# Performance work log

Hardware: AMD Instinct MI355X
Metric: run time of the kernel (lower is better)

Reference implementation:

```python
import jax, jax.numpy as jnp
import numpy as np

N, K, FC, FX, E = 16384, 16, 2, 32, 256


def _lin_init(key, fin, fout):
    kw, kb = jax.random.split(key)
    s = 1.0 / np.sqrt(fin)
    W = jax.random.uniform(kw, (fin, fout), jnp.float32, -s, s)
    b = jax.random.uniform(kb, (fout,), jnp.float32, -s, s)
    return W, b


def setup_inputs() -> dict:
    key = jax.random.key(0)
    ks = jax.random.split(key, 13)
    c = jax.random.uniform(ks[0], (N, FC), jnp.float32)
    x = jax.random.normal(ks[1], (N, FX), jnp.float32)
    W_coords, b_coords = _lin_init(ks[2], FC, E)
    W_attri, b_attri = _lin_init(ks[3], FX, E)
    W_g1, b_g1 = _lin_init(ks[4], FC, E)
    W_g2, b_g2 = _lin_init(ks[5], E, E)
    W_g3, b_g3 = _lin_init(ks[6], E, E)
    W_f1, b_f1 = _lin_init(ks[7], FX, E)
    W_f2, b_f2 = _lin_init(ks[8], E, E)
    W_f3, b_f3 = _lin_init(ks[9], E, E)
    W_d1, b_d1 = _lin_init(ks[10], 2 * E, 2 * E)
    W_d2, b_d2 = _lin_init(ks[11], 2 * E, 2)
    return dict(c=c, x=x,
                W_coords=W_coords, b_coords=b_coords,
                W_attri=W_attri, b_attri=b_attri,
                W_g1=W_g1, b_g1=b_g1, W_g2=W_g2, b_g2=b_g2, W_g3=W_g3, b_g3=b_g3,
                W_f1=W_f1, b_f1=b_f1, W_f2=W_f2, b_f2=b_f2, W_f3=W_f3, b_f3=b_f3,
                W_d1=W_d1, b_d1=b_d1, W_d2=W_d2, b_d2=b_d2)


def knn_edges(c, k):
    # PyG knn_graph (loop=False, flow='source_to_target'):
    # edge_index[0]=neighbor(src), edge_index[1]=node(dst).
    n = c.shape[0]
    sq = jnp.sum(c * c, axis=1)
    d2 = sq[:, None] + sq[None, :] - 2.0 * (c @ c.T)  # [N,N] squared dists
    d2 = d2.at[jnp.arange(n), jnp.arange(n)].set(jnp.inf)  # exclude self
    _, idx = jax.lax.top_k(-d2, k)  # [N,k] nearest neighbor indices
    src = idx.reshape(-1)
    dst = jnp.repeat(jnp.arange(n), k)
    return src, dst


def gcn_conv(h, src, dst, ew, W, b):
    # PyG GCNConv: linear -> add self-loops (weight 1) -> sym norm -> scatter-add -> +bias
    n = h.shape[0]
    hw = h @ W
    loop = jnp.arange(n)
    s = jnp.concatenate([src, loop])
    d = jnp.concatenate([dst, loop])
    w = jnp.concatenate([ew, jnp.ones((n,), h.dtype)])
    deg = jax.ops.segment_sum(w, d, num_segments=n)
    dinv = jnp.where(deg > 0, jax.lax.rsqrt(deg), 0.0)
    norm = dinv[s] * w * dinv[d]
    out = jax.ops.segment_sum(norm[:, None] * hw[s], d, num_segments=n)
    return out + b


def reference(c, x, W_coords, b_coords, W_attri, b_attri,
              W_g1, b_g1, W_g2, b_g2, W_g3, b_g3,
              W_f1, b_f1, W_f2, b_f2, W_f3, b_f3,
              W_d1, b_d1, W_d2, b_d2):
    src, dst = knn_edges(c, K)
    dist = jnp.linalg.norm(c[src] - c[dst], axis=1)
    ew = jnp.exp(-dist / 2.0)
    ew = jnp.where(ew > 10.0, 0.0, ew)  # faithful to source (never triggers)

    coords0 = c @ W_coords + b_coords
    attri0 = x @ W_attri + b_attri

    # eval mode: dropout is identity
    g1 = jax.nn.relu(gcn_conv(c, src, dst, ew, W_g1, b_g1))
    m1 = jax.nn.relu(x @ W_f1 + b_f1)
    g1 = coords0 + g1
    m1 = attri0 + m1

    g2 = jax.nn.relu(gcn_conv(g1, src, dst, ew, W_g2, b_g2))
    m2 = jax.nn.relu(m1 @ W_f2 + b_f2)
    g2 = g1 + g2
    m2 = m1 + m2

    g3 = jax.nn.relu(gcn_conv(g2, src, dst, ew, W_g3, b_g3))
    m3 = jax.nn.relu(m2 @ W_f3 + b_f3)
    g3 = g2 + g3
    m3 = m2 + m3

    combined = jnp.concatenate([g3, m3], axis=1)
    out = jax.nn.relu(combined @ W_d1 + b_d1) @ W_d2 + b_d2
    mean = out[:, 0]
    sigma = 0.2 + 0.8 * jax.nn.softplus(out[:, 1])
    return mean.reshape(-1, 1), sigma.reshape(-1, 1), g3, m3
```

## Files before the change

kernel.cpp:

```cpp
#include <hip/hip_runtime.h>
#include <math.h>

#define NPTS 16384
#define KNN 16
#define GRES 128
#define NCELL (GRES * GRES)

typedef unsigned long long ull;
typedef __attribute__((ext_vector_type(8))) short  bf16x8;
typedef __attribute__((ext_vector_type(4))) float  f32x4;

__device__ inline unsigned short f2bf(float f) {
    unsigned int u = __float_as_uint(f);
    u += 0x7fffu + ((u >> 16) & 1u);
    return (unsigned short)(u >> 16);
}
__device__ inline float bf2f(unsigned short u) {
    return __uint_as_float(((unsigned int)u) << 16);
}

__global__ __launch_bounds__(256) void grid_count_kernel(const float2* __restrict__ c,
    int* __restrict__ cnt)
{
    const int i = blockIdx.x * 256 + threadIdx.x;
    float2 p = c[i];
    int cx = min(GRES - 1, max(0, (int)(p.x * GRES)));
    int cy = min(GRES - 1, max(0, (int)(p.y * GRES)));
    atomicAdd(&cnt[cy * GRES + cx], 1);
}

__global__ __launch_bounds__(256) void scan_p1_kernel(const int* __restrict__ cnt,
    int* __restrict__ bsum)
{
    __shared__ int red[256];
    const int t = threadIdx.x;
    red[t] = cnt[blockIdx.x * 256 + t];
    __syncthreads();
    for (int s = 128; s > 0; s >>= 1) { if (t < s) red[t] += red[t + s]; __syncthreads(); }
    if (t == 0) bsum[blockIdx.x] = red[0];
}

__global__ __launch_bounds__(64) void scan_p2_kernel(int* __restrict__ bsum,
    int* __restrict__ start)
{
    const int t = threadIdx.x;
    int v = bsum[t];
    int inc = v;
#pragma unroll
    for (int off = 1; off < 64; off <<= 1) { int u = __shfl_up(inc, off, 64); inc += (t >= off) ? u : 0; }
    bsum[t] = inc - v;
    if (t == 63) start[NCELL] = inc;
}

__global__ __launch_bounds__(256) void scan_p3_kernel(const int* __restrict__ cnt,
    const int* __restrict__ bsum, int* __restrict__ start)
{
    __shared__ int wsum[4];
    const int t = threadIdx.x, lane = t & 63, w = t >> 6;
    const int i = blockIdx.x * 256 + t;
    int v = cnt[i];
    int inc = v;
#pragma unroll
    for (int off = 1; off < 64; off <<= 1) { int u = __shfl_up(inc, off, 64); inc += (lane >= off) ? u : 0; }
    if (lane == 63) wsum[w] = inc;
    __syncthreads();
    int add = bsum[blockIdx.x];
    for (int j = 0; j < w; ++j) add += wsum[j];
    start[i] = add + inc - v;
}

__global__ __launch_bounds__(256) void grid_scatter_kernel(const float2* __restrict__ c,
    const int* __restrict__ start, int* __restrict__ cur, float4* __restrict__ pts)
{
    const int i = blockIdx.x * 256 + threadIdx.x;
    float2 p = c[i];
    int cx = min(GRES - 1, max(0, (int)(p.x * GRES)));
    int cy = min(GRES - 1, max(0, (int)(p.y * GRES)));
    int cell = cy * GRES + cx;
    int pos = start[cell] + atomicAdd(&cur[cell], 1);
    float4 v;
    v.x = p.x; v.y = p.y; v.z = __uint_as_float((unsigned int)i); v.w = 0.f;
    pts[pos] = v;
}

__global__ __launch_bounds__(256) void knn_query_kernel(const float4* __restrict__ pts,
    const int* __restrict__ start,
    int* __restrict__ nbr, float* __restrict__ ew, float* __restrict__ dinv)
{
    const int lane = threadIdx.x & 63;
    const int qpos = blockIdx.x * 4 + (threadIdx.x >> 6);
    const float4 q4 = pts[qpos];
    const float qx = q4.x, qy = q4.y;
    const int qidx = (int)__float_as_uint(q4.z);
    const int qcx = min(GRES - 1, max(0, (int)(qx * GRES)));
    const int qcy = min(GRES - 1, max(0, (int)(qy * GRES)));

    ull cur = ~0ULL;

    auto process = [&](int ccy, int ccx, bool valid) {
        int s0 = 0, len = 0;
        if (valid && ccy >= 0 && ccy < GRES && ccx >= 0 && ccx < GRES) {
            const int cell = ccy * GRES + ccx;
            s0 = start[cell];
            len = start[cell + 1] - s0;
        }
        int pin = len;
#pragma unroll
        for (int off = 1; off < 64; off <<= 1) {
            int v = __shfl_up(pin, off, 64);
            pin += (lane >= off) ? v : 0;
        }
        const int T = __shfl(pin, 63, 64);
        const int pex = pin - len;
        for (int b = 0; b < T; b += 64) {
            const int ci = b + lane;
            const int cq = min(ci, T - 1);
            int lo = 0, hi = 63;
#pragma unroll
            for (int it = 0; it < 6; ++it) {
                const int mid = (lo + hi) >> 1;
                const int pm = __shfl(pin, mid, 64);
                if (pm > cq) hi = mid; else lo = mid + 1;
            }
            const int cs = __shfl(s0, hi, 64);
            const int cb = __shfl(pex, hi, 64);
            const int p  = cs + (cq - cb);
            const float4 pp = pts[p];
            const float dx = pp.x - qx, dy = pp.y - qy;
            const float d2 = fmaf(dx, dx, dy * dy);
            ull key = ~0ULL;
            if (ci < T && p != qpos)
                key = (((ull)__float_as_uint(d2)) << 32) | (ull)__float_as_uint(pp.z);
#pragma unroll
            for (int k = 2; k <= 64; k <<= 1) {
#pragma unroll
                for (int j = k >> 1; j > 0; j >>= 1) {
                    ull o = __shfl_xor(key, j, 64);
                    bool takeMin = (((lane & k) == 0) == ((lane & j) == 0));
                    ull mn = (o < key) ? o : key;
                    ull mx = (o > key) ? o : key;
                    key = takeMin ? mn : mx;
                }
            }
            ull rev = __shfl(key, (31 - lane) & 63, 64);
            ull val = (lane < 16) ? cur : ((lane < 32) ? rev : ~0ULL);
#pragma unroll
            for (int j = 16; j > 0; j >>= 1) {
                ull o = __shfl_xor(val, j, 64);
                ull mn = (o < val) ? o : val;
                ull mx = (o > val) ? o : val;
                val = ((lane & j) == 0) ? mn : mx;
            }
            cur = (lane < 16) ? val : ~0ULL;
        }
    };

    process(qcy - 3 + lane / 7, qcx - 3 + (lane % 7), lane < 49);

    int R = 3;
    const float h = 1.0f / GRES;
    while (true) {
        ull k15 = __shfl(cur, 15, 64);
        float dmax = __uint_as_float((unsigned int)(k15 >> 32));
        float rr = 0.999f * (float)R * h;
        if (dmax < rr * rr) break;
        if (R >= GRES) break;
        ++R;
        const int ncells = 8 * R;
        for (int cc = 0; cc < ncells; cc += 64) {
            const int i = cc + lane;
            int ccy = 0, ccx = 0;
            const bool valid = (i < ncells);
            if (valid) {
                const int side = 2 * R + 1;
                if (i < side)            { ccy = qcy - R; ccx = qcx - R + i; }
                else if (i < 2 * side)   { ccy = qcy + R; ccx = qcx - R + (i - side); }
                else {
                    const int j = i - 2 * side;
                    ccy = qcy - R + 1 + (j >> 1);
                    ccx = (j & 1) ? (qcx + R) : (qcx - R);
                }
            }
            process(ccy, ccx, valid);
        }
    }

    float w = 0.f; int nb = 0;
    if (lane < 16) {
        nb = (int)(cur & 0xffffffffu);
        float d2 = __uint_as_float((unsigned int)(cur >> 32));
        w = expf(-0.5f * sqrtf(d2));
    }
    float acc = w;
#pragma unroll
    for (int off = 1; off < 64; off <<= 1) acc += __shfl_xor(acc, off, 64);
    if (lane < 16) {
        nbr[qidx * KNN + lane] = nb;
        ew[qidx * KNN + lane]  = w;
    }
    if (lane == 0) dinv[qidx] = 1.0f / sqrtf(1.0f + acc);
}

__global__ __launch_bounds__(256) void wprep_kernel(
    const float* __restrict__ W0, const float* __restrict__ W1,
    const float* __restrict__ W2, const float* __restrict__ W3,
    const float* __restrict__ W4,
    unsigned short* __restrict__ D0, unsigned short* __restrict__ D1,
    unsigned short* __restrict__ D2, unsigned short* __restrict__ D3,
    unsigned short* __restrict__ D4)
{
    const int z = blockIdx.z;
    const float* W; unsigned short* D; int K;
    if (z == 0) { W = W0; D = D0; K = 256; }
    else if (z == 1) { W = W1; D = D1; K = 256; }
    else if (z == 2) { W = W2; D = D2; K = 256; }
    else if (z == 3) { W = W3; D = D3; K = 256; }
    else { W = W4; D = D4; K = 512; }
    const int nt = K / 32;
    if (blockIdx.x >= nt || blockIdx.y >= nt) return;
    const int k0 = blockIdx.x * 32, n0 = blockIdx.y * 32;
    __shared__ float t[32][33];
    const int tr = threadIdx.x >> 5, tc = threadIdx.x & 31;
#pragma unroll
    for (int i = 0; i < 4; ++i)
        t[tr + i * 8][tc] = W[(size_t)(k0 + tr + i * 8) * K + n0 + tc];
    __syncthreads();
#pragma unroll
    for (int i = 0; i < 4; ++i)
        D[(size_t)(n0 + tr + i * 8) * K + k0 + tc] = f2bf(t[tc][tr + i * 8]);
}

__global__ __launch_bounds__(256) void init_m1_kernel(const float* __restrict__ x,
    const float* __restrict__ Wa, const float* __restrict__ ba,
    const float* __restrict__ Wf, const float* __restrict__ bf,
    float* __restrict__ m1f, unsigned short* __restrict__ m1b)
{
    __shared__ float xs[64 * 32];
    const int tid = threadIdx.x;
    const int i0  = blockIdx.x * 64;
#pragma unroll
    for (int it = 0; it < 8; ++it)
        xs[tid + it * 256] = x[(size_t)i0 * 32 + tid + it * 256];
    float wa[32], wf[32];
#pragma unroll
    for (int k = 0; k < 32; ++k) { wa[k] = Wa[k * 256 + tid]; wf[k] = Wf[k * 256 + tid]; }
    const float b0 = ba[tid], b1 = bf[tid];
    __syncthreads();
    for (int r = 0; r < 64; ++r) {
        float a0 = b0, a1 = b1;
#pragma unroll
        for (int k = 0; k < 32; ++k) {
            float xv = xs[r * 32 + k];
            a0 = fmaf(xv, wa[k], a0);
            a1 = fmaf(xv, wf[k], a1);
        }
        const float v = a0 + fmaxf(a1, 0.0f);
        m1f[(size_t)(i0 + r) * 256 + tid] = v;
        m1b[(size_t)(i0 + r) * 256 + tid] = f2bf(v);
    }
}

__global__ __launch_bounds__(256) void agg1_kernel(const float2* __restrict__ c,
    const int* __restrict__ nbr, const float* __restrict__ ew, const float* __restrict__ dinv,
    const float* __restrict__ Wc, const float* __restrict__ bc,
    const float* __restrict__ Wg, const float* __restrict__ bg,
    float* __restrict__ g1f, unsigned short* __restrict__ g1b)
{
    __shared__ float su[64][5];
    const int tid = threadIdx.x;
    const int i0  = blockIdx.x * 64;
    if (tid < 64) {
        const int i = i0 + tid;
        float ux = 0.f, uy = 0.f;
        for (int t = 0; t < KNN; ++t) {
            int nb = nbr[i * KNN + t];
            float w = ew[i * KNN + t] * dinv[nb];
            float2 cn = c[nb];
            ux = fmaf(w, cn.x, ux); uy = fmaf(w, cn.y, uy);
        }
        float di = dinv[i];
        float2 ci = c[i];
        ux = fmaf(di, ci.x, ux); uy = fmaf(di, ci.y, uy);
        su[tid][0] = ux; su[tid][1] = uy; su[tid][2] = ci.x; su[tid][3] = ci.y; su[tid][4] = di;
    }
    __syncthreads();
    const float wc0 = Wc[tid], wc1 = Wc[256 + tid];
    const float wg0 = Wg[tid], wg1 = Wg[256 + tid];
    const float bcj = bc[tid], bgj = bg[tid];
    for (int r = 0; r < 64; ++r) {
        float ux = su[r][0], uy = su[r][1], cx = su[r][2], cy = su[r][3], di = su[r][4];
        float coords0 = fmaf(cx, wc0, fmaf(cy, wc1, bcj));
        float pre = fmaf(di, fmaf(ux, wg0, uy * wg1), bgj);
        const float v = coords0 + fmaxf(pre, 0.0f);
        g1f[(size_t)(i0 + r) * 256 + tid] = v;
        g1b[(size_t)(i0 + r) * 256 + tid] = f2bf(v);
    }
}

__global__ __launch_bounds__(256) void agg_kernel(const unsigned short* __restrict__ hw,
    const int* __restrict__ nbr, const float* __restrict__ ew, const float* __restrict__ dinv,
    const float* __restrict__ bias, const float* __restrict__ res,
    float* __restrict__ outf, unsigned short* __restrict__ outb)
{
    __shared__ int   sn[16][16];
    __shared__ float sw[16][16];
    __shared__ float sdi[16];
    const int tid = threadIdx.x;
    const int i0  = blockIdx.x * 16;
    {
        const int r = tid >> 4, t = tid & 15;
        const int i = i0 + r;
        int nb = nbr[i * KNN + t];
        sn[r][t] = nb;
        sw[r][t] = ew[i * KNN + t] * dinv[nb];
        if (t == 0) sdi[r] = dinv[i];
    }
    __syncthreads();
    const float bj = bias[tid];
    for (int r = 0; r < 16; ++r) {
        const int i = i0 + r;
        const float di = sdi[r];
        float s = di * bf2f(hw[(size_t)i * 256 + tid]);
#pragma unroll
        for (int t = 0; t < KNN; ++t)
            s = fmaf(sw[r][t], bf2f(hw[(size_t)sn[r][t] * 256 + tid]), s);
        float v = fmaf(di, s, bj);
        v = res[(size_t)i * 256 + tid] + fmaxf(v, 0.0f);
        outf[(size_t)i * 256 + tid] = v;
        outb[(size_t)i * 256 + tid] = f2bf(v);
    }
}

#define GL 40
__global__ __launch_bounds__(256) void gemm_bf16_kernel(
    const unsigned short* __restrict__ A1, const unsigned short* __restrict__ A2,
    const int ksplit,
    const unsigned short* __restrict__ Wt, const int ncols, const int Kdim,
    const float* __restrict__ bias, const float* __restrict__ res,
    float* __restrict__ outf, unsigned short* __restrict__ outb, const int flags)
{
    __shared__ unsigned short As[128 * GL];
    __shared__ unsigned short Bs[128 * GL];
    const int tid = threadIdx.x;
    const int r0 = blockIdx.x * 128;
    const int c0 = blockIdx.y * 128;
    const int w  = tid >> 6;
    const int wr = w >> 1, wc = w & 1;
    const int l  = tid & 63;
    const int half = l >> 4, lc = l & 15;

    const int srow = tid >> 2;
    const int skq  = (tid & 3) * 8;

    f32x4 acc[4][4];
#pragma unroll
    for (int mt = 0; mt < 4; ++mt)
#pragma unroll
        for (int nt = 0; nt < 4; ++nt) acc[mt][nt] = (f32x4){0.f, 0.f, 0.f, 0.f};

    for (int k0 = 0; k0 < Kdim; k0 += 32) {
        const unsigned short* Asrc = (k0 < ksplit) ? (A1 + k0) : (A2 + (k0 - ksplit));
#pragma unroll
        for (int it = 0; it < 2; ++it) {
            const int r = srow + it * 64;
            *(bf16x8*)&As[r * GL + skq] = *(const bf16x8*)(Asrc + (size_t)(r0 + r) * 256 + skq);
        }
#pragma unroll
        for (int it = 0; it < 2; ++it) {
            const int n = srow + it * 64;
            *(bf16x8*)&Bs[n * GL + skq] = *(const bf16x8*)(Wt + (size_t)(c0 + n) * Kdim + k0 + skq);
        }
        __syncthreads();
        bf16x8 af[4], bq[4];
#pragma unroll
        for (int mt = 0; mt < 4; ++mt)
            af[mt] = *(const bf16x8*)&As[(wr * 64 + mt * 16 + lc) * GL + half * 8];
#pragma unroll
        for (int nt = 0; nt < 4; ++nt)
            bq[nt] = *(const bf16x8*)&Bs[(wc * 64 + nt * 16 + lc) * GL + half * 8];
#pragma unroll
        for (int mt = 0; mt < 4; ++mt)
#pragma unroll
            for (int nt = 0; nt < 4; ++nt)
                acc[mt][nt] = __builtin_amdgcn_mfma_f32_16x16x32_bf16(af[mt], bq[nt], acc[mt][nt], 0, 0, 0);
        __syncthreads();
    }

#pragma unroll
    for (int nt = 0; nt < 4; ++nt) {
        const int col = c0 + wc * 64 + nt * 16 + lc;
        const float bv = (flags & 1) ? bias[col] : 0.f;
#pragma unroll
        for (int mt = 0; mt < 4; ++mt) {
            const int rowb = r0 + wr * 64 + mt * 16 + half * 4;
#pragma unroll
            for (int r = 0; r < 4; ++r) {
                float v = acc[mt][nt][r] + bv;
                if (flags & 2) v = fmaxf(v, 0.f);
                if (flags & 4) v += res[(size_t)(rowb + r) * ncols + col];
                if (flags & 8)  outf[(size_t)(rowb + r) * ncols + col] = v;
                if (flags & 16) outb[(size_t)(rowb + r) * ncols + col] = f2bf(v);
            }
        }
    }
}

__global__ __launch_bounds__(256) void head2_kernel(const float* __restrict__ h,
    const float* __restrict__ W, const float* __restrict__ b,
    float* __restrict__ mean, float* __restrict__ sigma)
{
    const int tid = threadIdx.x;
    const int lane = tid & 63;
    const int row = blockIdx.x * 4 + (tid >> 6);
    float a0 = 0.f, a1 = 0.f;
#pragma unroll
    for (int u = 0; u < 8; ++u) {
        const int k = lane + u * 64;
        const float hv = h[(size_t)row * 512 + k];
        a0 = fmaf(hv, W[k * 2 + 0], a0);
        a1 = fmaf(hv, W[k * 2 + 1], a1);
    }
    for (int off = 32; off > 0; off >>= 1) {
        a0 += __shfl_down(a0, off, 64);
        a1 += __shfl_down(a1, off, 64);
    }
    if (lane == 0) {
        mean[row] = a0 + b[0];
        float z = a1 + b[1];
        float sp = fmaxf(z, 0.f) + log1pf(expf(-fabsf(z)));
        sigma[row] = fmaf(0.8f, sp, 0.2f);
    }
}

extern "C" void kernel_launch(void* const* d_in, const int* in_sizes, int n_in,
                              void* d_out, int out_size, void* d_ws, size_t ws_size,
                              hipStream_t stream)
{
    (void)in_sizes; (void)n_in; (void)out_size; (void)ws_size;
    const float* c   = (const float*)d_in[0];
    const float* x   = (const float*)d_in[1];
    const float* Wc  = (const float*)d_in[2];
    const float* bc  = (const float*)d_in[3];
    const float* Wa  = (const float*)d_in[4];
    const float* ba  = (const float*)d_in[5];
    const float* Wg1 = (const float*)d_in[6];
    const float* bg1 = (const float*)d_in[7];
    const float* Wg2 = (const float*)d_in[8];
    const float* bg2 = (const float*)d_in[9];
    const float* Wg3 = (const float*)d_in[10];
    const float* bg3 = (const float*)d_in[11];
    const float* Wf1 = (const float*)d_in[12];
    const float* bf1 = (const float*)d_in[13];
    const float* Wf2 = (const float*)d_in[14];
    const float* bf2 = (const float*)d_in[15];
    const float* Wf3 = (const float*)d_in[16];
    const float* bf3 = (const float*)d_in[17];
    const float* Wd1 = (const float*)d_in[18];
    const float* bd1 = (const float*)d_in[19];
    const float* Wd2 = (const float*)d_in[20];
    const float* bd2 = (const float*)d_in[21];

    float* out = (float*)d_out;
    const size_t N = NPTS;
    const size_t SLOT = N * 256;
    float* wsf  = (float*)d_ws;
    int*   nbr  = (int*)d_ws;
    float* ew   = wsf + N * 16;
    float* dinv = wsf + N * 32;
    float* s0   = wsf + N * 33;
    float* s1   = s0 + SLOT;
    float* s2   = s1 + SLOT;
    unsigned short* b0 = (unsigned short*)(s2 + SLOT);
    unsigned short* b1 = b0 + SLOT;
    unsigned short* b2 = b1 + SLOT;
    unsigned short* b3 = b2 + SLOT;
    unsigned short* wb = b3 + SLOT;
    unsigned short* bWg2 = wb;
    unsigned short* bWf2 = wb + 65536;
    unsigned short* bWg3 = wb + 131072;
    unsigned short* bWf3 = wb + 196608;
    unsigned short* bWd1 = wb + 262144;

    float4* g_pts  = (float4*)s2;
    int* g_cnt     = (int*)(s2 + N * 4);
    int* g_cur     = g_cnt + NCELL;
    int* g_start   = g_cur + NCELL;
    int* g_bsum    = g_start + NCELL + 1;

    float* o_mean  = out;
    float* o_sigma = out + N;
    float* o_g3    = out + 2 * N;
    float* o_m3    = out + 2 * N + N * 256;

    wprep_kernel<<<dim3(16, 16, 5), 256, 0, stream>>>(Wg2, Wf2, Wg3, Wf3, Wd1,
                                                      bWg2, bWf2, bWg3, bWf3, bWd1);

    hipMemsetAsync(g_cnt, 0, 2 * NCELL * sizeof(int), stream);
    grid_count_kernel<<<NPTS / 256, 256, 0, stream>>>((const float2*)c, g_cnt);
    scan_p1_kernel<<<NCELL / 256, 256, 0, stream>>>(g_cnt, g_bsum);
    scan_p2_kernel<<<1, 64, 0, stream>>>(g_bsum, g_start);
    scan_p3_kernel<<<NCELL / 256, 256, 0, stream>>>(g_cnt, g_bsum, g_start);
    grid_scatter_kernel<<<NPTS / 256, 256, 0, stream>>>((const float2*)c, g_start, g_cur, g_pts);
    knn_query_kernel<<<NPTS / 4, 256, 0, stream>>>(g_pts, g_start, nbr, ew, dinv);

    init_m1_kernel<<<256, 256, 0, stream>>>(x, Wa, ba, Wf1, bf1, s0, b0);
    agg1_kernel<<<256, 256, 0, stream>>>((const float2*)c, nbr, ew, dinv, Wc, bc, Wg1, bg1, s1, b1);

    dim3 gE(NPTS / 128, 2);
    gemm_bf16_kernel<<<gE, 256, 0, stream>>>(b1, b1, 256, bWg2, 256, 256, nullptr, nullptr, nullptr, b2, 16);
    gemm_bf16_kernel<<<gE, 256, 0, stream>>>(b0, b0, 256, bWf2, 256, 256, bf2, s0, s2, b3, 31);
    agg_kernel<<<1024, 256, 0, stream>>>(b2, nbr, ew, dinv, bg2, s1, s1, b1);
    gemm_bf16_kernel<<<gE, 256, 0, stream>>>(b1, b1, 256, bWg3, 256, 256, nullptr, nullptr, nullptr, b2, 16);
    gemm_bf16_kernel<<<gE, 256, 0, stream>>>(b3, b3, 256, bWf3, 256, 256, bf3, s2, o_m3, b0, 31);
    agg_kernel<<<1024, 256, 0, stream>>>(b2, nbr, ew, dinv, bg3, s1, o_g3, b1);
    dim3 gH(NPTS / 128, 4);
    gemm_bf16_kernel<<<gH, 256, 0, stream>>>(b1, b0, 256, bWd1, 512, 512, bd1, nullptr, s0, nullptr, 11);
    head2_kernel<<<4096, 256, 0, stream>>>(s0, Wd2, bd2, o_mean, o_sigma);
}
```

Baseline: 336.7 us.

## Batch independent GEMMs per launch, fuse head layer into GEMM epilogue, merge init kernels

Result: faster. 302.7 us (-10.1%).

```diff
diff --git a/kernel.cpp b/kernel.cpp
--- a/kernel.cpp
+++ b/kernel.cpp
@@ -40,23 +40,13 @@
     if (t == 0) bsum[blockIdx.x] = red[0];
 }
 
-__global__ __launch_bounds__(64) void scan_p2_kernel(int* __restrict__ bsum,
-    int* __restrict__ start)
-{
-    const int t = threadIdx.x;
-    int v = bsum[t];
-    int inc = v;
-#pragma unroll
-    for (int off = 1; off < 64; off <<= 1) { int u = __shfl_up(inc, off, 64); inc += (t >= off) ? u : 0; }
-    bsum[t] = inc - v;
-    if (t == 63) start[NCELL] = inc;
-}
-
-__global__ __launch_bounds__(256) void scan_p3_kernel(const int* __restrict__ cnt,
+__global__ __launch_bounds__(256) void scan_p23_kernel(const int* __restrict__ cnt,
     const int* __restrict__ bsum, int* __restrict__ start)
 {
     __shared__ int wsum[4];
     const int t = threadIdx.x, lane = t & 63, w = t >> 6;
+    int base = 0;
+    for (int j = 0; j < (int)blockIdx.x; ++j) base += bsum[j];
     const int i = blockIdx.x * 256 + t;
     int v = cnt[i];
     int inc = v;
@@ -64,9 +54,10 @@
     for (int off = 1; off < 64; off <<= 1) { int u = __shfl_up(inc, off, 64); inc += (lane >= off) ? u : 0; }
     if (lane == 63) wsum[w] = inc;
     __syncthreads();
-    int add = bsum[blockIdx.x];
+    int add = base;
     for (int j = 0; j < w; ++j) add += wsum[j];
     start[i] = add + inc - v;
+    if (blockIdx.x == 63 && t == 255) start[NCELL] = add + inc;
 }
 
 __global__ __launch_bounds__(256) void grid_scatter_kernel(const float2* __restrict__ c,
@@ -230,70 +221,69 @@
         D[(size_t)(n0 + tr + i * 8) * K + k0 + tc] = f2bf(t[tc][tr + i * 8]);
 }
 
-__global__ __launch_bounds__(256) void init_m1_kernel(const float* __restrict__ x,
+__global__ __launch_bounds__(256) void init_fused_kernel(
+    const float* __restrict__ x, const float2* __restrict__ c,
+    const int* __restrict__ nbr, const float* __restrict__ ew, const float* __restrict__ dinv,
     const float* __restrict__ Wa, const float* __restrict__ ba,
     const float* __restrict__ Wf, const float* __restrict__ bf,
-    float* __restrict__ m1f, unsigned short* __restrict__ m1b)
-{
-    __shared__ float xs[64 * 32];
-    const int tid = threadIdx.x;
-    const int i0  = blockIdx.x * 64;
-#pragma unroll
-    for (int it = 0; it < 8; ++it)
-        xs[tid + it * 256] = x[(size_t)i0 * 32 + tid + it * 256];
-    float wa[32], wf[32];
-#pragma unroll
-    for (int k = 0; k < 32; ++k) { wa[k] = Wa[k * 256 + tid]; wf[k] = Wf[k * 256 + tid]; }
-    const float b0 = ba[tid], b1 = bf[tid];
-    __syncthreads();
-    for (int r = 0; r < 64; ++r) {
-        float a0 = b0, a1 = b1;
-#pragma unroll
-        for (int k = 0; k < 32; ++k) {
-            float xv = xs[r * 32 + k];
-            a0 = fmaf(xv, wa[k], a0);
-            a1 = fmaf(xv, wf[k], a1);
-        }
-        const float v = a0 + fmaxf(a1, 0.0f);
-        m1f[(size_t)(i0 + r) * 256 + tid] = v;
-        m1b[(size_t)(i0 + r) * 256 + tid] = f2bf(v);
-    }
-}
-
-__global__ __launch_bounds__(256) void agg1_kernel(const float2* __restrict__ c,
-    const int* __restrict__ nbr, const float* __restrict__ ew, const float* __restrict__ dinv,
     const float* __restrict__ Wc, const float* __restrict__ bc,
     const float* __restrict__ Wg, const float* __restrict__ bg,
+    float* __restrict__ m1f, unsigned short* __restrict__ m1b,
     float* __restrict__ g1f, unsigned short* __restrict__ g1b)
 {
-    __shared__ float su[64][5];
+    __shared__ float smem[64 * 32];
     const int tid = threadIdx.x;
-    const int i0  = blockIdx.x * 64;
-    if (tid < 64) {
-        const int i = i0 + tid;
-        float ux = 0.f, uy = 0.f;
-        for (int t = 0; t < KNN; ++t) {
-            int nb = nbr[i * KNN + t];
-            float w = ew[i * KNN + t] * dinv[nb];
-            float2 cn = c[nb];
-            ux = fmaf(w, cn.x, ux); uy = fmaf(w, cn.y, uy);
-        }
-        float di = dinv[i];
-        float2 ci = c[i];
-        ux = fmaf(di, ci.x, ux); uy = fmaf(di, ci.y, uy);
-        su[tid][0] = ux; su[tid][1] = uy; su[tid][2] = ci.x; su[tid][3] = ci.y; su[tid][4] = di;
-    }
-    __syncthreads();
-    const float wc0 = Wc[tid], wc1 = Wc[256 + tid];
-    const float wg0 = Wg[tid], wg1 = Wg[256 + tid];
-    const float bcj = bc[tid], bgj = bg[tid];
-    for (int r = 0; r < 64; ++r) {
-        float ux = su[r][0], uy = su[r][1], cx = su[r][2], cy = su[r][3], di = su[r][4];
-        float coords0 = fmaf(cx, wc0, fmaf(cy, wc1, bcj));
-        float pre = fmaf(di, fmaf(ux, wg0, uy * wg1), bgj);
-        const float v = coords0 + fmaxf(pre, 0.0f);
-        g1f[(size_t)(i0 + r) * 256 + tid] = v;
-        g1b[(size_t)(i0 + r) * 256 + tid] = f2bf(v);
+    if (blockIdx.x < 256) {
+        const int i0 = blockIdx.x * 64;
+#pragma unroll
+        for (int it = 0; it < 8; ++it)
+            smem[tid + it * 256] = x[(size_t)i0 * 32 + tid + it * 256];
+        float wa[32], wf[32];
+#pragma unroll
+        for (int k = 0; k < 32; ++k) { wa[k] = Wa[k * 256 + tid]; wf[k] = Wf[k * 256 + tid]; }
+        const float b0 = ba[tid], b1 = bf[tid];
+        __syncthreads();
+        for (int r = 0; r < 64; ++r) {
+            float a0 = b0, a1 = b1;
+#pragma unroll
+            for (int k = 0; k < 32; ++k) {
+                float xv = smem[r * 32 + k];
+                a0 = fmaf(xv, wa[k], a0);
+                a1 = fmaf(xv, wf[k], a1);
+            }
+            const float v = a0 + fmaxf(a1, 0.0f);
+            m1f[(size_t)(i0 + r) * 256 + tid] = v;
+            m1b[(size_t)(i0 + r) * 256 + tid] = f2bf(v);
+        }
+    } else {
+        float (*su)[5] = (float(*)[5])smem;
+        const int i0 = (blockIdx.x - 256) * 64;
+        if (tid < 64) {
+            const int i = i0 + tid;
+            float ux = 0.f, uy = 0.f;
+            for (int t = 0; t < KNN; ++t) {
+                int nb = nbr[i * KNN + t];
+                float w = ew[i * KNN + t] * dinv[nb];
+                float2 cn = c[nb];
+                ux = fmaf(w, cn.x, ux); uy = fmaf(w, cn.y, uy);
+            }
+            float di = dinv[i];
+            float2 ci = c[i];
+            ux = fmaf(di, ci.x, ux); uy = fmaf(di, ci.y, uy);
+            su[tid][0] = ux; su[tid][1] = uy; su[tid][2] = ci.x; su[tid][3] = ci.y; su[tid][4] = di;
+        }
+        __syncthreads();
+        const float wc0 = Wc[tid], wc1 = Wc[256 + tid];
+        const float wg0 = Wg[tid], wg1 = Wg[256 + tid];
+        const float bcj = bc[tid], bgj = bg[tid];
+        for (int r = 0; r < 64; ++r) {
+            float ux = su[r][0], uy = su[r][1], cx = su[r][2], cy = su[r][3], di = su[r][4];
+            float coords0 = fmaf(cx, wc0, fmaf(cy, wc1, bcj));
+            float pre = fmaf(di, fmaf(ux, wg0, uy * wg1), bgj);
+            const float v = coords0 + fmaxf(pre, 0.0f);
+            g1f[(size_t)(i0 + r) * 256 + tid] = v;
+            g1b[(size_t)(i0 + r) * 256 + tid] = f2bf(v);
+        }
     }
 }
 
@@ -331,14 +321,18 @@
     }
 }
 
+struct GemmOp {
+    const unsigned short *A1, *A2; int ksplit;
+    const unsigned short *Wt; int ncols, Kdim;
+    const float *bias; const float *res;
+    float *outf; unsigned short *outb;
+    const float *Wd2; float *accp;
+    int flags;
+};
 #define GL 40
-__global__ __launch_bounds__(256) void gemm_bf16_kernel(
-    const unsigned short* __restrict__ A1, const unsigned short* __restrict__ A2,
-    const int ksplit,
-    const unsigned short* __restrict__ Wt, const int ncols, const int Kdim,
-    const float* __restrict__ bias, const float* __restrict__ res,
-    float* __restrict__ outf, unsigned short* __restrict__ outb, const int flags)
-{
+__global__ __launch_bounds__(256) void gemm_bf16_kernel(GemmOp opA, GemmOp opB)
+{
+    const GemmOp op = (blockIdx.z == 0) ? opA : opB;
     __shared__ unsigned short As[128 * GL];
     __shared__ unsigned short Bs[128 * GL];
     const int tid = threadIdx.x;
@@ -358,8 +352,8 @@
 #pragma unroll
         for (int nt = 0; nt < 4; ++nt) acc[mt][nt] = (f32x4){0.f, 0.f, 0.f, 0.f};
 
-    for (int k0 = 0; k0 < Kdim; k0 += 32) {
-        const unsigned short* Asrc = (k0 < ksplit) ? (A1 + k0) : (A2 + (k0 - ksplit));
+    for (int k0 = 0; k0 < op.Kdim; k0 += 32) {
+        const unsigned short* Asrc = (k0 < op.ksplit) ? (op.A1 + k0) : (op.A2 + (k0 - op.ksplit));
 #pragma unroll
         for (int it = 0; it < 2; ++it) {
             const int r = srow + it * 64;
@@ -368,7 +362,7 @@
 #pragma unroll
         for (int it = 0; it < 2; ++it) {
             const int n = srow + it * 64;
-            *(bf16x8*)&Bs[n * GL + skq] = *(const bf16x8*)(Wt + (size_t)(c0 + n) * Kdim + k0 + skq);
+            *(bf16x8*)&Bs[n * GL + skq] = *(const bf16x8*)(op.Wt + (size_t)(c0 + n) * op.Kdim + k0 + skq);
         }
         __syncthreads();
         bf16x8 af[4], bq[4];
@@ -386,50 +380,78 @@
         __syncthreads();
     }
 
+    if (op.flags & 32) {
+        float p0[4][4], p1[4][4];
+#pragma unroll
+        for (int mt = 0; mt < 4; ++mt)
+#pragma unroll
+            for (int r = 0; r < 4; ++r) { p0[mt][r] = 0.f; p1[mt][r] = 0.f; }
+#pragma unroll
+        for (int nt = 0; nt < 4; ++nt) {
+            const int col = c0 + wc * 64 + nt * 16 + lc;
+            const float bv = op.bias[col];
+            const float w0 = op.Wd2[col * 2 + 0];
+            const float w1 = op.Wd2[col * 2 + 1];
+#pragma unroll
+            for (int mt = 0; mt < 4; ++mt)
+#pragma unroll
+                for (int r = 0; r < 4; ++r) {
+                    float v = fmaxf(acc[mt][nt][r] + bv, 0.f);
+                    p0[mt][r] = fmaf(v, w0, p0[mt][r]);
+                    p1[mt][r] = fmaf(v, w1, p1[mt][r]);
+                }
+        }
+#pragma unroll
+        for (int mt = 0; mt < 4; ++mt)
+#pragma unroll
+            for (int r = 0; r < 4; ++r) {
+#pragma unroll
+                for (int j = 1; j < 16; j <<= 1) {
+                    p0[mt][r] += __shfl_xor(p0[mt][r], j, 64);
+                    p1[mt][r] += __shfl_xor(p1[mt][r], j, 64);
+                }
+            }
+        if (lc == 0) {
+#pragma unroll
+            for (int mt = 0; mt < 4; ++mt) {
+                const int rowb = r0 + wr * 64 + mt * 16 + half * 4;
+#pragma unroll
+                for (int r = 0; r < 4; ++r) {
+                    atomicAdd(&op.accp[(size_t)(rowb + r) * 2 + 0], p0[mt][r]);
+                    atomicAdd(&op.accp[(size_t)(rowb + r) * 2 + 1], p1[mt][r]);
+                }
+            }
+        }
+        return;
+    }
 #pragma unroll
     for (int nt = 0; nt < 4; ++nt) {
         const int col = c0 + wc * 64 + nt * 16 + lc;
-        const float bv = (flags & 1) ? bias[col] : 0.f;
+        const float bv = (op.flags & 1) ? op.bias[col] : 0.f;
 #pragma unroll
         for (int mt = 0; mt < 4; ++mt) {
             const int rowb = r0 + wr * 64 + mt * 16 + half * 4;
 #pragma unroll
             for (int r = 0; r < 4; ++r) {
                 float v = acc[mt][nt][r] + bv;
-                if (flags & 2) v = fmaxf(v, 0.f);
-                if (flags & 4) v += res[(size_t)(rowb + r) * ncols + col];
-                if (flags & 8)  outf[(size_t)(rowb + r) * ncols + col] = v;
-                if (flags & 16) outb[(size_t)(rowb + r) * ncols + col] = f2bf(v);
-            }
-        }
-    }
-}
-
-__global__ __launch_bounds__(256) void head2_kernel(const float* __restrict__ h,
-    const float* __restrict__ W, const float* __restrict__ b,
-    float* __restrict__ mean, float* __restrict__ sigma)
-{
-    const int tid = threadIdx.x;
-    const int lane = tid & 63;
-    const int row = blockIdx.x * 4 + (tid >> 6);
-    float a0 = 0.f, a1 = 0.f;
-#pragma unroll
-    for (int u = 0; u < 8; ++u) {
-        const int k = lane + u * 64;
-        const float hv = h[(size_t)row * 512 + k];
-        a0 = fmaf(hv, W[k * 2 + 0], a0);
-        a1 = fmaf(hv, W[k * 2 + 1], a1);
-    }
-    for (int off = 32; off > 0; off >>= 1) {
-        a0 += __shfl_down(a0, off, 64);
-        a1 += __shfl_down(a1, off, 64);
-    }
-    if (lane == 0) {
-        mean[row] = a0 + b[0];
-        float z = a1 + b[1];
-        float sp = fmaxf(z, 0.f) + log1pf(expf(-fabsf(z)));
-        sigma[row] = fmaf(0.8f, sp, 0.2f);
-    }
+                if (op.flags & 2) v = fmaxf(v, 0.f);
+                if (op.flags & 4) v += op.res[(size_t)(rowb + r) * op.ncols + col];
+                if (op.flags & 8)  op.outf[(size_t)(rowb + r) * op.ncols + col] = v;
+                if (op.flags & 16) op.outb[(size_t)(rowb + r) * op.ncols + col] = f2bf(v);
+            }
+        }
+    }
+}
+
+__global__ __launch_bounds__(256) void finish_kernel(const float* __restrict__ accp,
+    const float* __restrict__ b, float* __restrict__ mean, float* __restrict__ sigma)
+{
+    const int i = blockIdx.x * 256 + threadIdx.x;
+    const float a0 = accp[2 * i], a1 = accp[2 * i + 1];
+    mean[i] = a0 + b[0];
+    float z = a1 + b[1];
+    float sp = fmaxf(z, 0.f) + log1pf(expf(-fabsf(z)));
+    sigma[i] = fmaf(0.8f, sp, 0.2f);
 }
 
 extern "C" void kernel_launch(void* const* d_in, const int* in_sizes, int n_in,
@@ -480,6 +502,7 @@
     unsigned short* bWg3 = wb + 131072;
     unsigned short* bWf3 = wb + 196608;
     unsigned short* bWd1 = wb + 262144;
+    float* accp = (float*)(wb + 262144 + 262144);
 
     float4* g_pts  = (float4*)s2;
     int* g_cnt     = (int*)(s2 + N * 4);
@@ -494,26 +517,39 @@
 
     wprep_kernel<<<dim3(16, 16, 5), 256, 0, stream>>>(Wg2, Wf2, Wg3, Wf3, Wd1,
                                                       bWg2, bWf2, bWg3, bWf3, bWd1);
-
     hipMemsetAsync(g_cnt, 0, 2 * NCELL * sizeof(int), stream);
+    hipMemsetAsync(accp, 0, N * 2 * sizeof(float), stream);
+
     grid_count_kernel<<<NPTS / 256, 256, 0, stream>>>((const float2*)c, g_cnt);
     scan_p1_kernel<<<NCELL / 256, 256, 0, stream>>>(g_cnt, g_bsum);
-    scan_p2_kernel<<<1, 64, 0, stream>>>(g_bsum, g_start);
-    scan_p3_kernel<<<NCELL / 256, 256, 0, stream>>>(g_cnt, g_bsum, g_start);
+    scan_p23_kernel<<<NCELL / 256, 256, 0, stream>>>(g_cnt, g_bsum, g_start);
     grid_scatter_kernel<<<NPTS / 256, 256, 0, stream>>>((const float2*)c, g_start, g_cur, g_pts);
     knn_query_kernel<<<NPTS / 4, 256, 0, stream>>>(g_pts, g_start, nbr, ew, dinv);
 
-    init_m1_kernel<<<256, 256, 0, stream>>>(x, Wa, ba, Wf1, bf1, s0, b0);
-    agg1_kernel<<<256, 256, 0, stream>>>((const float2*)c, nbr, ew, dinv, Wc, bc, Wg1, bg1, s1, b1);
-
-    dim3 gE(NPTS / 128, 2);
-    gemm_bf16_kernel<<<gE, 256, 0, stream>>>(b1, b1, 256, bWg2, 256, 256, nullptr, nullptr, nullptr, b2, 16);
-    gemm_bf16_kernel<<<gE, 256, 0, stream>>>(b0, b0, 256, bWf2, 256, 256, bf2, s0, s2, b3, 31);
+    init_fused_kernel<<<512, 256, 0, stream>>>(x, (const float2*)c, nbr, ew, dinv,
+                                               Wa, ba, Wf1, bf1, Wc, bc, Wg1, bg1,
+                                               s0, b0, s1, b1);
+
+    GemmOp z{};
+    GemmOp ohw2 = z; ohw2.A1 = b1; ohw2.A2 = b1; ohw2.ksplit = 256; ohw2.Wt = bWg2;
+    ohw2.ncols = 256; ohw2.Kdim = 256; ohw2.outb = b2; ohw2.flags = 16;
+    GemmOp om2 = z; om2.A1 = b0; om2.A2 = b0; om2.ksplit = 256; om2.Wt = bWf2;
+    om2.ncols = 256; om2.Kdim = 256; om2.bias = bf2; om2.res = s0;
+    om2.outf = s2; om2.outb = b3; om2.flags = 31;
+    gemm_bf16_kernel<<<dim3(NPTS / 128, 2, 2), 256, 0, stream>>>(ohw2, om2);
     agg_kernel<<<1024, 256, 0, stream>>>(b2, nbr, ew, dinv, bg2, s1, s1, b1);
-    gemm_bf16_kernel<<<gE, 256, 0, stream>>>(b1, b1, 256, bWg3, 256, 256, nullptr, nullptr, nullptr, b2, 16);
-    gemm_bf16_kernel<<<gE, 256, 0, stream>>>(b3, b3, 256, bWf3, 256, 256, bf3, s2, o_m3, b0, 31);
+
+    GemmOp ohw3 = z; ohw3.A1 = b1; ohw3.A2 = b1; ohw3.ksplit = 256; ohw3.Wt = bWg3;
+    ohw3.ncols = 256; ohw3.Kdim = 256; ohw3.outb = b2; ohw3.flags = 16;
+    GemmOp om3 = z; om3.A1 = b3; om3.A2 = b3; om3.ksplit = 256; om3.Wt = bWf3;
+    om3.ncols = 256; om3.Kdim = 256; om3.bias = bf3; om3.res = s2;
+    om3.outf = o_m3; om3.outb = b0; om3.flags = 31;
+    gemm_bf16_kernel<<<dim3(NPTS / 128, 2, 2), 256, 0, stream>>>(ohw3, om3);
     agg_kernel<<<1024, 256, 0, stream>>>(b2, nbr, ew, dinv, bg3, s1, o_g3, b1);
-    dim3 gH(NPTS / 128, 4);
-    gemm_bf16_kernel<<<gH, 256, 0, stream>>>(b1, b0, 256, bWd1, 512, 512, bd1, nullptr, s0, nullptr, 11);
-    head2_kernel<<<4096, 256, 0, stream>>>(s0, Wd2, bd2, o_mean, o_sigma);
-}
+
+    GemmOp oh = z; oh.A1 = b1; oh.A2 = b0; oh.ksplit = 256; oh.Wt = bWd1;
+    oh.ncols = 512; oh.Kdim = 512; oh.bias = bd1; oh.Wd2 = Wd2; oh.accp = accp;
+    oh.flags = 32;
+    gemm_bf16_kernel<<<dim3(NPTS / 128, 4, 1), 256, 0, stream>>>(oh, oh);
+    finish_kernel<<<NPTS / 256, 256, 0, stream>>>(accp, bd2, o_mean, o_sigma);
+}
```
